# Performance work log

Measured on AMD Instinct MI355X. Metric: run time of the kernel, lower is better.

The kernel has to match this reference:

```python
import jax, jax.numpy as jnp
import numpy as np

NUM_ITERATIONS = 3

def _squash(t, axis=-1):
    # norm here is the SQUARED norm, matching the torch code exactly
    norm = jnp.sum(t * t, axis=axis, keepdims=True)
    scale = norm / (1.0 + norm)
    return scale * t / jnp.sqrt(norm)

def setup_inputs() -> dict:
    key = jax.random.key(0)
    k1, k2 = jax.random.split(key)
    B, R, Cin = 1024, 2336, 4  # batch, num_routes, primary_capslen
    K, Cout = 2, 16            # num_caps, digital_capslen
    u = jax.random.normal(k1, (B, R, Cin), dtype=jnp.float32)
    W = jax.random.normal(k2, (K, R, Cin, Cout), dtype=jnp.float32)
    return {"u": u, "W": W}

def reference(u, W):
    # u: [B,R,Cin]; W: [K,R,Cin,Cout]
    # torch: u[:,None,:,None,:] @ W -> [B,K,R,1,Cout]; we drop the singleton.
    u_ji = jnp.einsum('bri,krio->bkro', u, W)  # [B,K,R,Cout]
    B, K, R, Cout = u_ji.shape
    # b is constant along the Cout axis (zeros init + delta_b keepdim), so keep it [B,K,R,1]
    b = jnp.zeros((B, K, R, 1), dtype=u_ji.dtype)
    v = None
    for i in range(NUM_ITERATIONS):
        c = jax.nn.softmax(b, axis=2)                      # softmax over routes (dim=2)
        s = jnp.sum(c * u_ji, axis=2, keepdims=True)       # [B,K,1,Cout]
        v = _squash(s, axis=-1)                            # [B,K,1,Cout]
        if i != NUM_ITERATIONS - 1:
            delta_b = jnp.sum(u_ji * v, axis=-1, keepdims=True)  # [B,K,R,1]
            b = b + delta_b
    v = jnp.squeeze(v, axis=2)                             # [B,K,Cout]
    classes = jnp.sqrt(jnp.sum(v * v, axis=-1))            # [B,K]
    return jax.nn.softmax(classes, axis=-1)                # F.softmax default dim=1 on 2D
```

## Files before the change

kernel.cpp:

```cpp
#include <hip/hip_runtime.h>
#include <stdint.h>

#define RT    2336
#define RL    928
#define NSL2  8
#define NRS2  11
#define NTH   512
#define NBLK  1024
#define BATCH 1024
#define SH1   32.0f
#define SH2   64.0f

typedef float v2f __attribute__((ext_vector_type(2)));

__device__ __forceinline__ float blo(uint32_t v){ union {uint32_t u; float f;} x; x.u = v << 16;        return x.f; }
__device__ __forceinline__ float bhi(uint32_t v){ union {uint32_t u; float f;} x; x.u = v & 0xffff0000u; return x.f; }

__device__ __forceinline__ uint32_t cvtpk_bf16(float a, float b){
  uint32_t r;
  asm("v_cvt_pk_bf16_f32 %0, %1, %2" : "=v"(r) : "v"(a), "v"(b));
  return r;
}

__device__ __forceinline__ v2f pk_fma(v2f a, v2f b, v2f c){
  v2f d; asm("v_pk_fma_f32 %0, %1, %2, %3" : "=v"(d) : "v"(a), "v"(b), "v"(c));
  return d;
}
__device__ __forceinline__ v2f pk_mul(v2f a, v2f b){
  v2f d; asm("v_pk_mul_f32 %0, %1, %2" : "=v"(d) : "v"(a), "v"(b));
  return d;
}
__device__ __forceinline__ v2f pk_add(v2f a, v2f b){
  v2f d; asm("v_pk_add_f32 %0, %1, %2" : "=v"(d) : "v"(a), "v"(b));
  return d;
}

__device__ __forceinline__ float qsum4(float d){
  d += __int_as_float(__builtin_amdgcn_update_dpp(
         0, __float_as_int(d), 0xB1, 0xF, 0xF, true));
  d += __int_as_float(__builtin_amdgcn_update_dpp(
         0, __float_as_int(d), 0x4E, 0xF, 0xF, true));
  return d;
}

__device__ __forceinline__ void merge2(float4 aA, float lA, float4 aB, float lB,
                                       int tid, float (*red)[8][4][5],
                                       float (*vbuf)[16],
                                       bool last, float* outp){
  #pragma unroll
  for (int off = 32; off >= 4; off >>= 1){
    aA.x += __shfl_down(aA.x, off); aA.y += __shfl_down(aA.y, off);
    aA.z += __shfl_down(aA.z, off); aA.w += __shfl_down(aA.w, off);
    lA   += __shfl_down(lA,   off);
    aB.x += __shfl_down(aB.x, off); aB.y += __shfl_down(aB.y, off);
    aB.z += __shfl_down(aB.z, off); aB.w += __shfl_down(aB.w, off);
    lB   += __shfl_down(lB,   off);
  }
  const int lane = tid & 63, wid = tid >> 6;
  if (lane < 4){
    red[0][wid][lane][0] = lA;
    red[0][wid][lane][1] = aA.x; red[0][wid][lane][2] = aA.y;
    red[0][wid][lane][3] = aA.z; red[0][wid][lane][4] = aA.w;
    red[1][wid][lane][0] = lB;
    red[1][wid][lane][1] = aB.x; red[1][wid][lane][2] = aB.y;
    red[1][wid][lane][3] = aB.z; red[1][wid][lane][4] = aB.w;
  }
  __syncthreads();
  if (tid < 32){
    const int bt = tid >> 4, t = tid & 15, q = t >> 2, j = t & 3;
    float S = 0.f, partL = 0.f;
    #pragma unroll
    for (int w = 0; w < 8; ++w){
      S     += red[bt][w][q][1 + j];
      partL += red[bt][w][j][0];
    }
    partL += __shfl_xor(partL, 1);
    partL += __shfl_xor(partL, 2);
    float L   = partL * 0.25f;
    float inv = 1.f / L;
    float Sn  = S * inv;
    float nrm = Sn * Sn;
    nrm += __shfl_xor(nrm, 1);
    nrm += __shfl_xor(nrm, 2);
    nrm += __shfl_xor(nrm, 4);
    nrm += __shfl_xor(nrm, 8);
    if (last){
      if (t == 0) outp[bt << 1] = nrm / (1.f + nrm);
    } else {
      float f = sqrtf(nrm) / (1.f + nrm);
      vbuf[bt][t] = Sn * f;
    }
  }
  __syncthreads();
}

__global__ void __launch_bounds__(NTH, 2)
caps_route(const float* __restrict__ U, const float* __restrict__ W,
           float* __restrict__ Out){
  __shared__ uint4 uj4[RL * 4];
  __shared__ float red[2][8][4][5];
  __shared__ float vbuf[2][16];

  const int tid = threadIdx.x;
  const int qo  = tid & 3;

  const int c    = blockIdx.x & 7;
  const int jj   = blockIdx.x >> 3;
  const int k    = jj & 1;
  const int pair = (c << 6) | (jj >> 1);
  const int bb   = pair << 1;

  const float* Ub0 = U + (size_t)bb * (RT * 4);
  const float* Ub1 = Ub0 + (RT * 4);
  const float* Wk  = W + (size_t)k * ((size_t)RT * 64) + qo * 4;

  uint2  ura[NRS2], urb[NRS2];
  float  vA0, vA1, vA2, vA3, vB0, vB1, vB2, vB3;

  auto build2 = [&](int route, v2f& pa01, v2f& pa23, v2f& pb01, v2f& pb23){
    float4 ua = *(const float4*)(Ub0 + (size_t)route * 4);
    float4 ub = *(const float4*)(Ub1 + (size_t)route * 4);
    const float* wr = Wk + (size_t)route * 64;
    float4 w0 = *(const float4*)(wr);
    float4 w1 = *(const float4*)(wr + 16);
    float4 w2 = *(const float4*)(wr + 32);
    float4 w3 = *(const float4*)(wr + 48);
    v2f w0l = {w0.x,w0.y}, w0h = {w0.z,w0.w};
    v2f w1l = {w1.x,w1.y}, w1h = {w1.z,w1.w};
    v2f w2l = {w2.x,w2.y}, w2h = {w2.z,w2.w};
    v2f w3l = {w3.x,w3.y}, w3h = {w3.z,w3.w};
    v2f sa0 = {ua.x,ua.x}, sa1 = {ua.y,ua.y}, sa2 = {ua.z,ua.z}, sa3 = {ua.w,ua.w};
    v2f sb0 = {ub.x,ub.x}, sb1 = {ub.y,ub.y}, sb2 = {ub.z,ub.z}, sb3 = {ub.w,ub.w};
    pa01 = pk_mul(sa0, w0l);          pa23 = pk_mul(sa0, w0h);
    pa01 = pk_fma(sa1, w1l, pa01);    pa23 = pk_fma(sa1, w1h, pa23);
    pa01 = pk_fma(sa2, w2l, pa01);    pa23 = pk_fma(sa2, w2h, pa23);
    pa01 = pk_fma(sa3, w3l, pa01);    pa23 = pk_fma(sa3, w3h, pa23);
    pb01 = pk_mul(sb0, w0l);          pb23 = pk_mul(sb0, w0h);
    pb01 = pk_fma(sb1, w1l, pb01);    pb23 = pk_fma(sb1, w1h, pb23);
    pb01 = pk_fma(sb2, w2l, pb01);    pb23 = pk_fma(sb2, w2h, pb23);
    pb01 = pk_fma(sb3, w3l, pb01);    pb23 = pk_fma(sb3, w3h, pb23);
  };

  v2f accA01 = {0.f,0.f}, accA23 = {0.f,0.f};
  v2f accB01 = {0.f,0.f}, accB23 = {0.f,0.f};

  if (tid < 128){
    int route = tid >> 2;
    v2f pa01, pa23, pb01, pb23;
    build2(route, pa01, pa23, pb01, pb23);
    accA01 = pk_add(accA01, pa01); accA23 = pk_add(accA23, pa23);
    accB01 = pk_add(accB01, pb01); accB23 = pk_add(accB23, pb23);
    uj4[route*4 + qo] = make_uint4(
      cvtpk_bf16(pa01.x, pa01.y), cvtpk_bf16(pa23.x, pa23.y),
      cvtpk_bf16(pb01.x, pb01.y), cvtpk_bf16(pb23.x, pb23.y));
  }
  #pragma unroll 3
  for (int s = 0; s < 7; ++s){
    int route = 32 + s*128 + (tid >> 2);
    v2f pa01, pa23, pb01, pb23;
    build2(route, pa01, pa23, pb01, pb23);
    accA01 = pk_add(accA01, pa01); accA23 = pk_add(accA23, pa23);
    accB01 = pk_add(accB01, pb01); accB23 = pk_add(accB23, pb23);
    uj4[route*4 + qo] = make_uint4(
      cvtpk_bf16(pa01.x, pa01.y), cvtpk_bf16(pa23.x, pa23.y),
      cvtpk_bf16(pb01.x, pb01.y), cvtpk_bf16(pb23.x, pb23.y));
  }
  #pragma unroll
  for (int slot = 0; slot < NRS2; ++slot){
    int route = RL + slot*128 + (tid >> 2);
    v2f pa01, pa23, pb01, pb23;
    build2(route, pa01, pa23, pb01, pb23);
    accA01 = pk_add(accA01, pa01); accA23 = pk_add(accA23, pa23);
    accB01 = pk_add(accB01, pb01); accB23 = pk_add(accB23, pb23);
    ura[slot] = make_uint2(cvtpk_bf16(pa01.x, pa01.y), cvtpk_bf16(pa23.x, pa23.y));
    urb[slot] = make_uint2(cvtpk_bf16(pb01.x, pb01.y), cvtpk_bf16(pb23.x, pb23.y));
  }
  float lA = (tid < 128) ? 19.f : 18.f, lB = lA;
  merge2(make_float4(accA01.x, accA01.y, accA23.x, accA23.y), lA,
         make_float4(accB01.x, accB01.y, accB23.x, accB23.y), lB,
         tid, red, vbuf, false, nullptr);
  vA0 = vbuf[0][4*qo]; vA1 = vbuf[0][4*qo+1]; vA2 = vbuf[0][4*qo+2]; vA3 = vbuf[0][4*qo+3];
  vB0 = vbuf[1][4*qo]; vB1 = vbuf[1][4*qo+1]; vB2 = vbuf[1][4*qo+2]; vB3 = vbuf[1][4*qo+3];

  for (int ps = 0; ps < 2; ++ps){
    const float SH = ps ? SH2 : SH1;
    float4 accA = make_float4(0.f,0.f,0.f,0.f), accB = make_float4(0.f,0.f,0.f,0.f);
    float lpA = 0.f, lpB = 0.f;
    #pragma unroll
    for (int s = 0; s < NSL2; ++s){
      int idx = tid + (s << 9);
      bool act = (idx < RL * 4);
      float a0=0.f,a1=0.f,a2=0.f,a3=0.f, c0=0.f,c1=0.f,c2=0.f,c3=0.f;
      float dA = 0.f, dB = 0.f;
      if (act){
        uint4 q4 = uj4[idx];
        a0 = blo(q4.x); a1 = bhi(q4.x); a2 = blo(q4.y); a3 = bhi(q4.y);
        c0 = blo(q4.z); c1 = bhi(q4.z); c2 = blo(q4.w); c3 = bhi(q4.w);
        dA = fmaf(a0, vA0, fmaf(a1, vA1, fmaf(a2, vA2, a3 * vA3)));
        dB = fmaf(c0, vB0, fmaf(c1, vB1, fmaf(c2, vB2, c3 * vB3)));
      }
      dA = qsum4(dA); dB = qsum4(dB);
      if (act){
        float eA = __expf(dA - SH), eB = __expf(dB - SH);
        lpA += eA; lpB += eB;
        accA.x = fmaf(eA, a0, accA.x); accA.y = fmaf(eA, a1, accA.y);
        accA.z = fmaf(eA, a2, accA.z); accA.w = fmaf(eA, a3, accA.w);
        accB.x = fmaf(eB, c0, accB.x); accB.y = fmaf(eB, c1, accB.y);
        accB.z = fmaf(eB, c2, accB.z); accB.w = fmaf(eB, c3, accB.w);
      }
    }
    #pragma unroll
    for (int slot = 0; slot < NRS2; ++slot){
      uint2 qa = ura[slot], qb = urb[slot];
      float a0 = blo(qa.x), a1 = bhi(qa.x), a2 = blo(qa.y), a3 = bhi(qa.y);
      float c0 = blo(qb.x), c1 = bhi(qb.x), c2 = blo(qb.y), c3 = bhi(qb.y);
      float dA = fmaf(a0, vA0, fmaf(a1, vA1, fmaf(a2, vA2, a3 * vA3)));
      float dB = fmaf(c0, vB0, fmaf(c1, vB1, fmaf(c2, vB2, c3 * vB3)));
      dA = qsum4(dA); dB = qsum4(dB);
      float eA = __expf(dA - SH), eB = __expf(dB - SH);
      lpA += eA; lpB += eB;
      accA.x = fmaf(eA, a0, accA.x); accA.y = fmaf(eA, a1, accA.y);
      accA.z = fmaf(eA, a2, accA.z); accA.w = fmaf(eA, a3, accA.w);
      accB.x = fmaf(eB, c0, accB.x); accB.y = fmaf(eB, c1, accB.y);
      accB.z = fmaf(eB, c2, accB.z); accB.w = fmaf(eB, c3, accB.w);
    }
    merge2(accA, lpA, accB, lpB, tid, red, vbuf, ps == 1,
           Out + (bb << 1) + k);
    if (ps == 0){
      vA0 += vbuf[0][4*qo]; vA1 += vbuf[0][4*qo+1];
      vA2 += vbuf[0][4*qo+2]; vA3 += vbuf[0][4*qo+3];
      vB0 += vbuf[1][4*qo]; vB1 += vbuf[1][4*qo+1];
      vB2 += vbuf[1][4*qo+2]; vB3 += vbuf[1][4*qo+3];
    }
  }
}

__global__ void caps_softmax(float* __restrict__ Out){
  int b = blockIdx.x * blockDim.x + threadIdx.x;
  if (b < BATCH){
    float2* p = (float2*)Out;
    float2 c = p[b];
    float m  = fmaxf(c.x, c.y);
    float e0 = __expf(c.x - m), e1 = __expf(c.y - m);
    float inv = 1.f / (e0 + e1);
    p[b] = make_float2(e0 * inv, e1 * inv);
  }
}

extern "C" void kernel_launch(void* const* d_in, const int* in_sizes, int n_in,
                              void* d_out, int out_size, void* d_ws, size_t ws_size,
                              hipStream_t stream) {
  const float* U = (const float*)d_in[0];
  const float* W = (const float*)d_in[1];
  float* Out = (float*)d_out;
  caps_route<<<dim3(NBLK), dim3(NTH), 0, stream>>>(U, W, Out);
  caps_softmax<<<dim3(BATCH / 256), dim3(256), 0, stream>>>(Out);
}
```

Measured before the change: 133.1 us.

## Stage W through LDS with double-buffered async global_load_lds pipeline

Each block now loads W in 128-route chunks from global memory straight into shared memory using global_load_lds, double-buffered so the next chunk's transfer overlaps compute on the current one. U loads are prefetched one chunk ahead. The bf16 route cache is rebalanced: 1024 routes go to LDS and the rest to registers, with a tail of 32 routes handled separately, which removes the bounds checks in the routing loops. This adds 64KB of LDS and drops launch bounds to one block per CU, so occupancy is lower in exchange for better memory-latency hiding.

```diff
diff --git a/kernel.cpp b/kernel.cpp
--- a/kernel.cpp
+++ b/kernel.cpp
@@ -2,9 +2,10 @@
 #include <stdint.h>
 
 #define RT    2336
-#define RL    928
-#define NSL2  8
-#define NRS2  11
+#define RL    1024
+#define NCH   18
+#define NRS3  10
+#define NSL3  8
 #define NTH   512
 #define NBLK  1024
 #define BATCH 1024
@@ -94,90 +95,120 @@
   __syncthreads();
 }
 
-__global__ void __launch_bounds__(NTH, 2)
+__global__ void __launch_bounds__(NTH, 1)
 caps_route(const float* __restrict__ U, const float* __restrict__ W,
            float* __restrict__ Out){
   __shared__ uint4 uj4[RL * 4];
+  __shared__ float wst[2][8192];
   __shared__ float red[2][8][4][5];
   __shared__ float vbuf[2][16];
 
-  const int tid = threadIdx.x;
-  const int qo  = tid & 3;
-
-  const int c    = blockIdx.x & 7;
+  const int tid  = threadIdx.x;
+  const int qo   = tid & 3;
+  const int q    = tid >> 2;
+  const int wv   = tid >> 6;
+  const int lane = tid & 63;
+
+  const int c8   = blockIdx.x & 7;
   const int jj   = blockIdx.x >> 3;
   const int k    = jj & 1;
-  const int pair = (c << 6) | (jj >> 1);
+  const int pair = (c8 << 6) | (jj >> 1);
   const int bb   = pair << 1;
 
   const float* Ub0 = U + (size_t)bb * (RT * 4);
   const float* Ub1 = Ub0 + (RT * 4);
-  const float* Wk  = W + (size_t)k * ((size_t)RT * 64) + qo * 4;
-
-  uint2  ura[NRS2], urb[NRS2];
-  float  vA0, vA1, vA2, vA3, vB0, vB1, vB2, vB3;
-
-  auto build2 = [&](int route, v2f& pa01, v2f& pa23, v2f& pb01, v2f& pb23){
-    float4 ua = *(const float4*)(Ub0 + (size_t)route * 4);
-    float4 ub = *(const float4*)(Ub1 + (size_t)route * 4);
-    const float* wr = Wk + (size_t)route * 64;
+  const char*  Wb  = (const char*)W + (size_t)k * RT * 256;
+
+  uint2 ura[NRS3 + 1], urb[NRS3 + 1];
+  float vA0,vA1,vA2,vA3, vB0,vB1,vB2,vB3;
+
+  auto dma = [&](int c, int buf){
+    const char* g = Wb + ((size_t)c << 15) + (wv << 12) + (lane << 4);
+    char* l = (char*)&wst[buf][0] + (wv << 12);
+    #pragma unroll
+    for (int j = 0; j < 4; ++j)
+      __builtin_amdgcn_global_load_lds(
+        (const __attribute__((address_space(1))) uint32_t*)(g + (j << 10)),
+        (__attribute__((address_space(3))) uint32_t*)(l + (j << 10)),
+        16, 0, 0);
+  };
+
+  v2f accA01={0.f,0.f}, accA23={0.f,0.f}, accB01={0.f,0.f}, accB23={0.f,0.f};
+
+  dma(0, 0);
+
+  if (tid < 128){
+    int rt = 2304 + q;
+    float4 ua = *(const float4*)(Ub0 + (size_t)rt * 4);
+    float4 ub = *(const float4*)(Ub1 + (size_t)rt * 4);
+    const float* wr = (const float*)(Wb + (size_t)rt * 256) + (qo << 2);
     float4 w0 = *(const float4*)(wr);
     float4 w1 = *(const float4*)(wr + 16);
     float4 w2 = *(const float4*)(wr + 32);
     float4 w3 = *(const float4*)(wr + 48);
-    v2f w0l = {w0.x,w0.y}, w0h = {w0.z,w0.w};
-    v2f w1l = {w1.x,w1.y}, w1h = {w1.z,w1.w};
-    v2f w2l = {w2.x,w2.y}, w2h = {w2.z,w2.w};
-    v2f w3l = {w3.x,w3.y}, w3h = {w3.z,w3.w};
-    v2f sa0 = {ua.x,ua.x}, sa1 = {ua.y,ua.y}, sa2 = {ua.z,ua.z}, sa3 = {ua.w,ua.w};
-    v2f sb0 = {ub.x,ub.x}, sb1 = {ub.y,ub.y}, sb2 = {ub.z,ub.z}, sb3 = {ub.w,ub.w};
-    pa01 = pk_mul(sa0, w0l);          pa23 = pk_mul(sa0, w0h);
-    pa01 = pk_fma(sa1, w1l, pa01);    pa23 = pk_fma(sa1, w1h, pa23);
-    pa01 = pk_fma(sa2, w2l, pa01);    pa23 = pk_fma(sa2, w2h, pa23);
-    pa01 = pk_fma(sa3, w3l, pa01);    pa23 = pk_fma(sa3, w3h, pa23);
-    pb01 = pk_mul(sb0, w0l);          pb23 = pk_mul(sb0, w0h);
-    pb01 = pk_fma(sb1, w1l, pb01);    pb23 = pk_fma(sb1, w1h, pb23);
-    pb01 = pk_fma(sb2, w2l, pb01);    pb23 = pk_fma(sb2, w2h, pb23);
-    pb01 = pk_fma(sb3, w3l, pb01);    pb23 = pk_fma(sb3, w3h, pb23);
-  };
-
-  v2f accA01 = {0.f,0.f}, accA23 = {0.f,0.f};
-  v2f accB01 = {0.f,0.f}, accB23 = {0.f,0.f};
-
-  if (tid < 128){
-    int route = tid >> 2;
-    v2f pa01, pa23, pb01, pb23;
-    build2(route, pa01, pa23, pb01, pb23);
-    accA01 = pk_add(accA01, pa01); accA23 = pk_add(accA23, pa23);
-    accB01 = pk_add(accB01, pb01); accB23 = pk_add(accB23, pb23);
-    uj4[route*4 + qo] = make_uint4(
-      cvtpk_bf16(pa01.x, pa01.y), cvtpk_bf16(pa23.x, pa23.y),
-      cvtpk_bf16(pb01.x, pb01.y), cvtpk_bf16(pb23.x, pb23.y));
-  }
-  #pragma unroll 3
-  for (int s = 0; s < 7; ++s){
-    int route = 32 + s*128 + (tid >> 2);
-    v2f pa01, pa23, pb01, pb23;
-    build2(route, pa01, pa23, pb01, pb23);
-    accA01 = pk_add(accA01, pa01); accA23 = pk_add(accA23, pa23);
-    accB01 = pk_add(accB01, pb01); accB23 = pk_add(accB23, pb23);
-    uj4[route*4 + qo] = make_uint4(
-      cvtpk_bf16(pa01.x, pa01.y), cvtpk_bf16(pa23.x, pa23.y),
-      cvtpk_bf16(pb01.x, pb01.y), cvtpk_bf16(pb23.x, pb23.y));
-  }
+    v2f w0l={w0.x,w0.y}, w0h={w0.z,w0.w}, w1l={w1.x,w1.y}, w1h={w1.z,w1.w};
+    v2f w2l={w2.x,w2.y}, w2h={w2.z,w2.w}, w3l={w3.x,w3.y}, w3h={w3.z,w3.w};
+    v2f sa0={ua.x,ua.x}, sa1={ua.y,ua.y}, sa2={ua.z,ua.z}, sa3={ua.w,ua.w};
+    v2f sb0={ub.x,ub.x}, sb1={ub.y,ub.y}, sb2={ub.z,ub.z}, sb3={ub.w,ub.w};
+    v2f pa01 = pk_mul(sa0,w0l), pa23 = pk_mul(sa0,w0h);
+    pa01 = pk_fma(sa1,w1l,pa01); pa23 = pk_fma(sa1,w1h,pa23);
+    pa01 = pk_fma(sa2,w2l,pa01); pa23 = pk_fma(sa2,w2h,pa23);
+    pa01 = pk_fma(sa3,w3l,pa01); pa23 = pk_fma(sa3,w3h,pa23);
+    v2f pb01 = pk_mul(sb0,w0l), pb23 = pk_mul(sb0,w0h);
+    pb01 = pk_fma(sb1,w1l,pb01); pb23 = pk_fma(sb1,w1h,pb23);
+    pb01 = pk_fma(sb2,w2l,pb01); pb23 = pk_fma(sb2,w2h,pb23);
+    pb01 = pk_fma(sb3,w3l,pb01); pb23 = pk_fma(sb3,w3h,pb23);
+    accA01 = pk_add(accA01,pa01); accA23 = pk_add(accA23,pa23);
+    accB01 = pk_add(accB01,pb01); accB23 = pk_add(accB23,pb23);
+    ura[NRS3] = make_uint2(cvtpk_bf16(pa01.x,pa01.y), cvtpk_bf16(pa23.x,pa23.y));
+    urb[NRS3] = make_uint2(cvtpk_bf16(pb01.x,pb01.y), cvtpk_bf16(pb23.x,pb23.y));
+  }
+
+  float4 ua = *(const float4*)(Ub0 + (size_t)q * 4);
+  float4 ub = *(const float4*)(Ub1 + (size_t)q * 4);
+
   #pragma unroll
-  for (int slot = 0; slot < NRS2; ++slot){
-    int route = RL + slot*128 + (tid >> 2);
-    v2f pa01, pa23, pb01, pb23;
-    build2(route, pa01, pa23, pb01, pb23);
-    accA01 = pk_add(accA01, pa01); accA23 = pk_add(accA23, pa23);
-    accB01 = pk_add(accB01, pb01); accB23 = pk_add(accB23, pb23);
-    ura[slot] = make_uint2(cvtpk_bf16(pa01.x, pa01.y), cvtpk_bf16(pa23.x, pa23.y));
-    urb[slot] = make_uint2(cvtpk_bf16(pb01.x, pb01.y), cvtpk_bf16(pb23.x, pb23.y));
-  }
-  float lA = (tid < 128) ? 19.f : 18.f, lB = lA;
-  merge2(make_float4(accA01.x, accA01.y, accA23.x, accA23.y), lA,
-         make_float4(accB01.x, accB01.y, accB23.x, accB23.y), lB,
+  for (int c = 0; c < NCH; ++c){
+    __syncthreads();
+    if (c + 1 < NCH) dma(c + 1, (c + 1) & 1);
+    float4 cua = ua, cub = ub;
+    if (c + 1 < NCH){
+      int rn = ((c + 1) << 7) + q;
+      ua = *(const float4*)(Ub0 + (size_t)rn * 4);
+      ub = *(const float4*)(Ub1 + (size_t)rn * 4);
+    }
+    const float* wb = &wst[c & 1][(q << 6) + (qo << 2)];
+    float4 w0 = *(const float4*)(wb);
+    float4 w1 = *(const float4*)(wb + 16);
+    float4 w2 = *(const float4*)(wb + 32);
+    float4 w3 = *(const float4*)(wb + 48);
+    v2f w0l={w0.x,w0.y}, w0h={w0.z,w0.w}, w1l={w1.x,w1.y}, w1h={w1.z,w1.w};
+    v2f w2l={w2.x,w2.y}, w2h={w2.z,w2.w}, w3l={w3.x,w3.y}, w3h={w3.z,w3.w};
+    v2f sa0={cua.x,cua.x}, sa1={cua.y,cua.y}, sa2={cua.z,cua.z}, sa3={cua.w,cua.w};
+    v2f sb0={cub.x,cub.x}, sb1={cub.y,cub.y}, sb2={cub.z,cub.z}, sb3={cub.w,cub.w};
+    v2f pa01 = pk_mul(sa0,w0l), pa23 = pk_mul(sa0,w0h);
+    pa01 = pk_fma(sa1,w1l,pa01); pa23 = pk_fma(sa1,w1h,pa23);
+    pa01 = pk_fma(sa2,w2l,pa01); pa23 = pk_fma(sa2,w2h,pa23);
+    pa01 = pk_fma(sa3,w3l,pa01); pa23 = pk_fma(sa3,w3h,pa23);
+    v2f pb01 = pk_mul(sb0,w0l), pb23 = pk_mul(sb0,w0h);
+    pb01 = pk_fma(sb1,w1l,pb01); pb23 = pk_fma(sb1,w1h,pb23);
+    pb01 = pk_fma(sb2,w2l,pb01); pb23 = pk_fma(sb2,w2h,pb23);
+    pb01 = pk_fma(sb3,w3l,pb01); pb23 = pk_fma(sb3,w3h,pb23);
+    accA01 = pk_add(accA01,pa01); accA23 = pk_add(accA23,pa23);
+    accB01 = pk_add(accB01,pb01); accB23 = pk_add(accB23,pb23);
+    int route = (c << 7) + q;
+    if (c < 8){
+      uj4[(route << 2) + qo] = make_uint4(
+        cvtpk_bf16(pa01.x,pa01.y), cvtpk_bf16(pa23.x,pa23.y),
+        cvtpk_bf16(pb01.x,pb01.y), cvtpk_bf16(pb23.x,pb23.y));
+    } else {
+      ura[c - 8] = make_uint2(cvtpk_bf16(pa01.x,pa01.y), cvtpk_bf16(pa23.x,pa23.y));
+      urb[c - 8] = make_uint2(cvtpk_bf16(pb01.x,pb01.y), cvtpk_bf16(pb23.x,pb23.y));
+    }
+  }
+  float l0 = (tid < 128) ? 19.f : 18.f;
+  merge2(make_float4(accA01.x,accA01.y,accA23.x,accA23.y), l0,
+         make_float4(accB01.x,accB01.y,accB23.x,accB23.y), l0,
          tid, red, vbuf, false, nullptr);
   vA0 = vbuf[0][4*qo]; vA1 = vbuf[0][4*qo+1]; vA2 = vbuf[0][4*qo+2]; vA3 = vbuf[0][4*qo+3];
   vB0 = vbuf[1][4*qo]; vB1 = vbuf[1][4*qo+1]; vB2 = vbuf[1][4*qo+2]; vB3 = vbuf[1][4*qo+3];
@@ -187,30 +218,23 @@
     float4 accA = make_float4(0.f,0.f,0.f,0.f), accB = make_float4(0.f,0.f,0.f,0.f);
     float lpA = 0.f, lpB = 0.f;
     #pragma unroll
-    for (int s = 0; s < NSL2; ++s){
+    for (int s = 0; s < NSL3; ++s){
       int idx = tid + (s << 9);
-      bool act = (idx < RL * 4);
-      float a0=0.f,a1=0.f,a2=0.f,a3=0.f, c0=0.f,c1=0.f,c2=0.f,c3=0.f;
-      float dA = 0.f, dB = 0.f;
-      if (act){
-        uint4 q4 = uj4[idx];
-        a0 = blo(q4.x); a1 = bhi(q4.x); a2 = blo(q4.y); a3 = bhi(q4.y);
-        c0 = blo(q4.z); c1 = bhi(q4.z); c2 = blo(q4.w); c3 = bhi(q4.w);
-        dA = fmaf(a0, vA0, fmaf(a1, vA1, fmaf(a2, vA2, a3 * vA3)));
-        dB = fmaf(c0, vB0, fmaf(c1, vB1, fmaf(c2, vB2, c3 * vB3)));
-      }
+      uint4 q4 = uj4[idx];
+      float a0 = blo(q4.x), a1 = bhi(q4.x), a2 = blo(q4.y), a3 = bhi(q4.y);
+      float c0 = blo(q4.z), c1 = bhi(q4.z), c2 = blo(q4.w), c3 = bhi(q4.w);
+      float dA = fmaf(a0, vA0, fmaf(a1, vA1, fmaf(a2, vA2, a3 * vA3)));
+      float dB = fmaf(c0, vB0, fmaf(c1, vB1, fmaf(c2, vB2, c3 * vB3)));
       dA = qsum4(dA); dB = qsum4(dB);
-      if (act){
-        float eA = __expf(dA - SH), eB = __expf(dB - SH);
-        lpA += eA; lpB += eB;
-        accA.x = fmaf(eA, a0, accA.x); accA.y = fmaf(eA, a1, accA.y);
-        accA.z = fmaf(eA, a2, accA.z); accA.w = fmaf(eA, a3, accA.w);
-        accB.x = fmaf(eB, c0, accB.x); accB.y = fmaf(eB, c1, accB.y);
-        accB.z = fmaf(eB, c2, accB.z); accB.w = fmaf(eB, c3, accB.w);
-      }
-    }
-    #pragma unroll
-    for (int slot = 0; slot < NRS2; ++slot){
+      float eA = __expf(dA - SH), eB = __expf(dB - SH);
+      lpA += eA; lpB += eB;
+      accA.x = fmaf(eA, a0, accA.x); accA.y = fmaf(eA, a1, accA.y);
+      accA.z = fmaf(eA, a2, accA.z); accA.w = fmaf(eA, a3, accA.w);
+      accB.x = fmaf(eB, c0, accB.x); accB.y = fmaf(eB, c1, accB.y);
+      accB.z = fmaf(eB, c2, accB.z); accB.w = fmaf(eB, c3, accB.w);
+    }
+    #pragma unroll
+    for (int slot = 0; slot < NRS3; ++slot){
       uint2 qa = ura[slot], qb = urb[slot];
       float a0 = blo(qa.x), a1 = bhi(qa.x), a2 = blo(qa.y), a3 = bhi(qa.y);
       float c0 = blo(qb.x), c1 = bhi(qb.x), c2 = blo(qb.y), c3 = bhi(qb.y);
@@ -224,6 +248,20 @@
       accB.x = fmaf(eB, c0, accB.x); accB.y = fmaf(eB, c1, accB.y);
       accB.z = fmaf(eB, c2, accB.z); accB.w = fmaf(eB, c3, accB.w);
     }
+    if (tid < 128){
+      uint2 qa = ura[NRS3], qb = urb[NRS3];
+      float a0 = blo(qa.x), a1 = bhi(qa.x), a2 = blo(qa.y), a3 = bhi(qa.y);
+      float c0 = blo(qb.x), c1 = bhi(qb.x), c2 = blo(qb.y), c3 = bhi(qb.y);
+      float dA = fmaf(a0, vA0, fmaf(a1, vA1, fmaf(a2, vA2, a3 * vA3)));
+      float dB = fmaf(c0, vB0, fmaf(c1, vB1, fmaf(c2, vB2, c3 * vB3)));
+      dA = qsum4(dA); dB = qsum4(dB);
+      float eA = __expf(dA - SH), eB = __expf(dB - SH);
+      lpA += eA; lpB += eB;
+      accA.x = fmaf(eA, a0, accA.x); accA.y = fmaf(eA, a1, accA.y);
+      accA.z = fmaf(eA, a2, accA.z); accA.w = fmaf(eA, a3, accA.w);
+      accB.x = fmaf(eB, c0, accB.x); accB.y = fmaf(eB, c1, accB.y);
+      accB.z = fmaf(eB, c2, accB.z); accB.w = fmaf(eB, c3, accB.w);
+    }
     merge2(accA, lpA, accB, lpB, tid, red, vbuf, ps == 1,
            Out + (bb << 1) + k);
     if (ps == 0){
```

Result: slower. 161.5 us (+21.3%).
